# Optimization experiments

Measured on AMD Instinct MI355X. Metric: run time of the kernel, lower is better.

Reference implementation:

```python
import jax, jax.numpy as jnp
import numpy as np

HEADS = 8
DIM_HEAD = 8  # TransMIL passes heads as dim_head to NystromLayer
INNER = HEADS * DIM_HEAD  # 64
LANDMARKS = 256
PINV_ITERS = 6
HID = 512
IN_DIM = 1024
N_TOKENS = 19600


def layernorm(x, g, b, eps=1e-5):
    mu = x.mean(-1, keepdims=True)
    var = ((x - mu) ** 2).mean(-1, keepdims=True)
    return (x - mu) / jnp.sqrt(var + eps) * g + b


def moore_penrose_pinv(a, iters=PINV_ITERS):
    # a: [b, h, m, m]
    abs_a = jnp.abs(a)
    z = jnp.swapaxes(a, -1, -2) / (jnp.max(abs_a.sum(-1)) * jnp.max(abs_a.sum(-2)))
    I = jnp.eye(a.shape[-1], dtype=a.dtype)
    for _ in range(iters):
        az = a @ z
        z = 0.25 * z @ (13.0 * I - az @ (15.0 * I - az @ (7.0 * I - az)))
    return z


def dwconv2d(x, w, b, pad_h, pad_w):
    # x: [B,C,H,W], w: [C,1,kh,kw] depthwise
    y = jax.lax.conv_general_dilated(
        x, w, (1, 1), [(pad_h, pad_h), (pad_w, pad_w)],
        dimension_numbers=('NCHW', 'OIHW', 'NCHW'), feature_group_count=x.shape[1])
    if b is not None:
        y = y + b[None, :, None, None]
    return y


def nystrom_attention(x, qkv_w, out_w, out_b, res_w):
    b, n, _ = x.shape
    m = LANDMARKS
    pad = (m - n % m) % m
    xp = jnp.pad(x, ((0, 0), (pad, 0), (0, 0)))  # pad at the FRONT (as in lucidrains)
    n_p = n + pad
    qkv = xp @ qkv_w  # [b, n_p, 3*inner]
    q, k, v = jnp.split(qkv, 3, axis=-1)
    to_heads = lambda t: t.reshape(b, n_p, HEADS, DIM_HEAD).transpose(0, 2, 1, 3)
    q, k, v = to_heads(q), to_heads(k), to_heads(v)  # [b,h,n_p,d]
    q = q * (DIM_HEAD ** -0.5)
    l = n_p // m  # segment length per landmark
    q_l = q.reshape(b, HEADS, m, l, DIM_HEAD).mean(3)  # [b,h,m,d]
    k_l = k.reshape(b, HEADS, m, l, DIM_HEAD).mean(3)
    attn1 = jax.nn.softmax(jnp.einsum('bhid,bhjd->bhij', q, k_l), -1)    # [b,h,n_p,m]
    attn2 = jax.nn.softmax(jnp.einsum('bhid,bhjd->bhij', q_l, k_l), -1)  # [b,h,m,m]
    attn3 = jax.nn.softmax(jnp.einsum('bhid,bhjd->bhij', q_l, k), -1)    # [b,h,m,n_p]
    out = (attn1 @ moore_penrose_pinv(attn2)) @ (attn3 @ v)  # [b,h,n_p,d]
    # residual depthwise conv over sequence dim: Conv2d(heads, heads, (33,1), padding=(16,0), groups=heads)
    out = out + dwconv2d(v, res_w, None, 16, 0)
    out = out.transpose(0, 2, 1, 3).reshape(b, n_p, INNER)
    out = out @ out_w + out_b
    return out[:, -n:]


def ppeg(x, H, W, w7, b7, w5, b5, w3, b3):
    B, _, C = x.shape
    cls, feat = x[:, :1], x[:, 1:]
    f = feat.transpose(0, 2, 1).reshape(B, C, H, W)
    y = f + dwconv2d(f, w7, b7, 3, 3) + dwconv2d(f, w5, b5, 2, 2) + dwconv2d(f, w3, b3, 1, 1)
    y = y.reshape(B, C, H * W).transpose(0, 2, 1)
    return jnp.concatenate([cls, y], axis=1)


def transmil_forward(x, fc1_w, fc1_b, cls_token,
                     l1_norm_g, l1_norm_b, l1_qkv_w, l1_out_w, l1_out_b, l1_res_w,
                     l2_norm_g, l2_norm_b, l2_qkv_w, l2_out_w, l2_out_b, l2_res_w,
                     ppeg7_w, ppeg7_b, ppeg5_w, ppeg5_b, ppeg3_w, ppeg3_b,
                     norm_g, norm_b):
    h = jax.nn.gelu(x @ fc1_w + fc1_b, approximate=False)  # [1, N, HID]
    N = h.shape[1]
    side = int(np.ceil(np.sqrt(N)))
    add = side * side - N
    h = jnp.concatenate([h, h[:, :add]], axis=1)
    cls = jnp.broadcast_to(cls_token, (h.shape[0], 1, h.shape[2]))
    h = jnp.concatenate([cls, h], axis=1)
    h = h + nystrom_attention(layernorm(h, l1_norm_g, l1_norm_b), l1_qkv_w, l1_out_w, l1_out_b, l1_res_w)
    h = ppeg(h, side, side, ppeg7_w, ppeg7_b, ppeg5_w, ppeg5_b, ppeg3_w, ppeg3_b)
    h = h + nystrom_attention(layernorm(h, l2_norm_g, l2_norm_b), l2_qkv_w, l2_out_w, l2_out_b, l2_res_w)
    return layernorm(h, norm_g, norm_b)[:, 0]  # [1, HID]


def setup_inputs() -> dict:
    key = jax.random.key(0)
    ks = jax.random.split(key, 16)
    s = 0.02
    inp = {
        'x': jax.random.normal(ks[0], (1, N_TOKENS, IN_DIM), jnp.float32),
        'fc1_w': jax.random.normal(ks[1], (IN_DIM, HID), jnp.float32) * s,
        'fc1_b': jnp.zeros((HID,), jnp.float32),
        'cls_token': jax.random.normal(ks[2], (1, 1, HID), jnp.float32),
        'l1_norm_g': jnp.ones((HID,), jnp.float32),
        'l1_norm_b': jnp.zeros((HID,), jnp.float32),
        'l1_qkv_w': jax.random.normal(ks[3], (HID, 3 * INNER), jnp.float32) * s,
        'l1_out_w': jax.random.normal(ks[4], (INNER, HID), jnp.float32) * s,
        'l1_out_b': jnp.zeros((HID,), jnp.float32),
        'l1_res_w': jax.random.normal(ks[5], (HEADS, 1, 33, 1), jnp.float32) * 0.05,
        'l2_norm_g': jnp.ones((HID,), jnp.float32),
        'l2_norm_b': jnp.zeros((HID,), jnp.float32),
        'l2_qkv_w': jax.random.normal(ks[6], (HID, 3 * INNER), jnp.float32) * s,
        'l2_out_w': jax.random.normal(ks[7], (INNER, HID), jnp.float32) * s,
        'l2_out_b': jnp.zeros((HID,), jnp.float32),
        'l2_res_w': jax.random.normal(ks[8], (HEADS, 1, 33, 1), jnp.float32) * 0.05,
        'ppeg7_w': jax.random.normal(ks[9], (HID, 1, 7, 7), jnp.float32) * 0.05,
        'ppeg7_b': jnp.zeros((HID,), jnp.float32),
        'ppeg5_w': jax.random.normal(ks[10], (HID, 1, 5, 5), jnp.float32) * 0.05,
        'ppeg5_b': jnp.zeros((HID,), jnp.float32),
        'ppeg3_w': jax.random.normal(ks[11], (HID, 1, 3, 3), jnp.float32) * 0.05,
        'ppeg3_b': jnp.zeros((HID,), jnp.float32),
        'norm_g': jnp.ones((HID,), jnp.float32),
        'norm_b': jnp.zeros((HID,), jnp.float32),
    }
    return inp


def reference(x, fc1_w, fc1_b, cls_token,
              l1_norm_g, l1_norm_b, l1_qkv_w, l1_out_w, l1_out_b, l1_res_w,
              l2_norm_g, l2_norm_b, l2_qkv_w, l2_out_w, l2_out_b, l2_res_w,
              ppeg7_w, ppeg7_b, ppeg5_w, ppeg5_b, ppeg3_w, ppeg3_b,
              norm_g, norm_b):
    return transmil_forward(x, fc1_w, fc1_b, cls_token,
                            l1_norm_g, l1_norm_b, l1_qkv_w, l1_out_w, l1_out_b, l1_res_w,
                            l2_norm_g, l2_norm_b, l2_qkv_w, l2_out_w, l2_out_b, l2_res_w,
                            ppeg7_w, ppeg7_b, ppeg5_w, ppeg5_b, ppeg3_w, ppeg3_b,
                            norm_g, norm_b)
```

## Files before the change

### kernel.cpp

```cpp
#include <hip/hip_runtime.h>

namespace {

constexpr int NP   = 19712;
constexpr int NT   = 19601;
constexpr int NPIX = 19600;
constexpr int HD   = 512;
constexpr int ID   = 1024;
constexpr int NH   = 8;
constexpr int DH   = 8;
constexpr int NL   = 256;
constexpr int PADR = 111;
constexpr int SIDE = 140;
constexpr int CCH  = 128;
constexpr int PW   = 148;
constexpr int A3CHK = 256;
constexpr int A3NB  = NP / A3CHK;

typedef __attribute__((ext_vector_type(8))) short bf16x8;
typedef __attribute__((ext_vector_type(4))) float f32x4;

#define F4MAD(a, s, v) { (a).x += (s)*(v).x; (a).y += (s)*(v).y; (a).z += (s)*(v).z; (a).w += (s)*(v).w; }

#define GLOAD16(gptr, lptr) \
    __builtin_amdgcn_global_load_lds((const __attribute__((address_space(1))) void*)(gptr), \
                                     (__attribute__((address_space(3))) void*)(lptr), 16, 0, 0)

__device__ inline short f2bf(float f) {
    union { float f; unsigned u; } v; v.f = f;
    unsigned r = v.u + 0x7fffu + ((v.u >> 16) & 1u);
    return (short)(r >> 16);
}

__global__ void castX(const float* __restrict__ src, short* __restrict__ dst)
{
    size_t c = (size_t)blockIdx.x * 256 + threadIdx.x;
    const float4 x0 = *(const float4*)&src[c * 8];
    const float4 x1 = *(const float4*)&src[c * 8 + 4];
    bf16x8 p;
    p[0] = f2bf(x0.x); p[1] = f2bf(x0.y); p[2] = f2bf(x0.z); p[3] = f2bf(x0.w);
    p[4] = f2bf(x1.x); p[5] = f2bf(x1.y); p[6] = f2bf(x1.z); p[7] = f2bf(x1.w);
    *(bf16x8*)&dst[c * 8] = p;
}

__global__ void castT(const float* __restrict__ src, short* __restrict__ dst, int R, int C)
{
    __shared__ float t[32][33];
    const int tx = threadIdx.x & 31, ty = threadIdx.x >> 5;
    const int c0 = blockIdx.x * 32, r0 = blockIdx.y * 32;
    #pragma unroll
    for (int j = 0; j < 4; ++j)
        t[ty + 8 * j][tx] = src[(size_t)(r0 + ty + 8 * j) * C + c0 + tx];
    __syncthreads();
    #pragma unroll
    for (int j = 0; j < 4; ++j)
        dst[(size_t)(c0 + ty + 8 * j) * R + r0 + tx] = f2bf(t[tx][ty + 8 * j]);
}

__global__ __launch_bounds__(256) void gemm_fc1(const short* __restrict__ Xb,
                                                const short* __restrict__ Wt,
                                                const float* __restrict__ bias,
                                                float* __restrict__ out)
{
    __shared__ __align__(16) short As[2][128 * 32];
    __shared__ __align__(16) short Bs[2][128 * 32];
    const int tid  = threadIdx.x;
    const int col0 = blockIdx.x * 128;
    const int row0 = blockIdx.y * 128;
    const int wave = tid >> 6, lane = tid & 63;
    const int quad = lane >> 4, l16 = lane & 15;
    const int m_base = (wave >> 1) * 64, n_base = (wave & 1) * 64;
    const int kch = (quad ^ ((l16 >> 1) & 3)) * 8;
    f32x4 acc[4][4] = {};

    int    aldo[2];
    size_t agoff[2], bgoff[2];
    #pragma unroll
    for (int i = 0; i < 2; ++i) {
        int slot = i * 256 + wave * 64 + lane;
        int row  = slot >> 2;
        int g    = (slot & 3) ^ ((slot >> 3) & 3);
        aldo[i]  = slot * 8;
        agoff[i] = (size_t)(row0 + row) * ID + g * 8;
        bgoff[i] = (size_t)(col0 + row) * ID + g * 8;
    }
    auto stage = [&](int b, int k0) {
        #pragma unroll
        for (int i = 0; i < 2; ++i) {
            GLOAD16(&Xb[agoff[i] + k0], &As[b][aldo[i]]);
            GLOAD16(&Wt[bgoff[i] + k0], &Bs[b][aldo[i]]);
        }
    };

    stage(0, 0);
    __syncthreads();
    #pragma unroll 1
    for (int t = 0; t < 32; ++t) {
        const int cur = t & 1;
        if (t < 31) stage(cur ^ 1, (t + 1) * 32);
        bf16x8 af[4], bfr[4];
        #pragma unroll
        for (int i = 0; i < 4; ++i) {
            af[i]  = *(const bf16x8*)&As[cur][(m_base + i * 16 + l16) * 32 + kch];
            bfr[i] = *(const bf16x8*)&Bs[cur][(n_base + i * 16 + l16) * 32 + kch];
        }
        #pragma unroll
        for (int mi = 0; mi < 4; ++mi)
            #pragma unroll
            for (int ni = 0; ni < 4; ++ni)
                acc[mi][ni] = __builtin_amdgcn_mfma_f32_16x16x32_bf16(af[mi], bfr[ni], acc[mi][ni], 0, 0, 0);
        __syncthreads();
    }
    #pragma unroll
    for (int mi = 0; mi < 4; ++mi) {
        #pragma unroll
        for (int r = 0; r < 4; ++r) {
            int gr = row0 + m_base + mi * 16 + quad * 4 + r;
            if (gr >= NPIX) continue;
            #pragma unroll
            for (int ni = 0; ni < 4; ++ni) {
                int gc = col0 + n_base + ni * 16 + l16;
                float v = acc[mi][ni][r] + bias[gc];
                v = 0.5f * v * (1.f + erff(v * 0.70710678118654752f));
                out[(size_t)(gr + 1) * HD + gc] = v;
            }
        }
    }
}

__global__ __launch_bounds__(256) void gemm_qkv(const short* __restrict__ xpB,
                                                const short* __restrict__ Wt,
                                                float* __restrict__ qh,
                                                float* __restrict__ kh,
                                                float* __restrict__ vh)
{
    __shared__ __align__(16) short As[2][128 * 32];
    __shared__ __align__(16) short Bs[2][64 * 32];
    const int tid  = threadIdx.x;
    const int col0 = blockIdx.x * 64;
    const int row0 = blockIdx.y * 128;
    const int wave = tid >> 6, lane = tid & 63;
    const int quad = lane >> 4, l16 = lane & 15;
    const int m_base = (wave >> 1) * 64, n_base = (wave & 1) * 32;
    const int kch = (quad ^ ((l16 >> 1) & 3)) * 8;
    f32x4 acc[4][2] = {};

    int    aldo[2];
    size_t agoff[2];
    #pragma unroll
    for (int i = 0; i < 2; ++i) {
        int slot = i * 256 + wave * 64 + lane;
        int row  = slot >> 2;
        int g    = (slot & 3) ^ ((slot >> 3) & 3);
        aldo[i]  = slot * 8;
        agoff[i] = (size_t)(row0 + row) * HD + g * 8;
    }
    int bldo; size_t bgoff;
    {
        int slot = wave * 64 + lane;
        int row  = slot >> 2;
        int g    = (slot & 3) ^ ((slot >> 3) & 3);
        bldo  = slot * 8;
        bgoff = (size_t)(col0 + row) * HD + g * 8;
    }
    auto stage = [&](int b, int k0) {
        #pragma unroll
        for (int i = 0; i < 2; ++i)
            GLOAD16(&xpB[agoff[i] + k0], &As[b][aldo[i]]);
        GLOAD16(&Wt[bgoff + k0], &Bs[b][bldo]);
    };

    stage(0, 0);
    __syncthreads();
    #pragma unroll 1
    for (int t = 0; t < 16; ++t) {
        const int cur = t & 1;
        if (t < 15) stage(cur ^ 1, (t + 1) * 32);
        bf16x8 af[4], bfr[2];
        #pragma unroll
        for (int i = 0; i < 4; ++i)
            af[i] = *(const bf16x8*)&As[cur][(m_base + i * 16 + l16) * 32 + kch];
        #pragma unroll
        for (int i = 0; i < 2; ++i)
            bfr[i] = *(const bf16x8*)&Bs[cur][(n_base + i * 16 + l16) * 32 + kch];
        #pragma unroll
        for (int mi = 0; mi < 4; ++mi)
            #pragma unroll
            for (int ni = 0; ni < 2; ++ni)
                acc[mi][ni] = __builtin_amdgcn_mfma_f32_16x16x32_bf16(af[mi], bfr[ni], acc[mi][ni], 0, 0, 0);
        __syncthreads();
    }
    const int which = blockIdx.x;
    float* dst = (which == 0) ? qh : (which == 1) ? kh : vh;
    const float scale = (which == 0) ? 0.35355339059327373f : 1.f;
    #pragma unroll
    for (int mi = 0; mi < 4; ++mi) {
        #pragma unroll
        for (int r = 0; r < 4; ++r) {
            int gr = row0 + m_base + mi * 16 + quad * 4 + r;
            #pragma unroll
            for (int ni = 0; ni < 2; ++ni) {
                int n = n_base + ni * 16 + l16;
                int hh = n >> 3, d = n & 7;
                dst[((size_t)hh * NP + gr) * DH + d] = acc[mi][ni][r] * scale;
            }
        }
    }
}

__global__ void cls_init(const float* __restrict__ cls, float* __restrict__ h)
{
    int t = blockIdx.x * 256 + threadIdx.x;
    if (t < HD) h[t] = cls[t];
}

__global__ void copy512(const float* __restrict__ src, float* __restrict__ dst)
{
    dst[threadIdx.x] = src[threadIdx.x];
}

__global__ __launch_bounds__(256) void ln_pad(const float* __restrict__ h,
                                              const float* __restrict__ g,
                                              const float* __restrict__ b,
                                              short* __restrict__ xp)
{
    const int wave = threadIdx.x >> 6, lane = threadIdx.x & 63;
    const int row = blockIdx.x * 4 + wave;
    short* dst = xp + (size_t)row * HD + lane * 8;
    if (row < PADR) {
        bf16x8 z = {};
        *(bf16x8*)dst = z;
        return;
    }
    const float* src = h + (size_t)(row - PADR) * HD + lane * 8;
    float4 v0 = *(const float4*)src;
    float4 v1 = *(const float4*)(src + 4);
    float v[8] = {v0.x, v0.y, v0.z, v0.w, v1.x, v1.y, v1.z, v1.w};
    float s = 0.f;
    #pragma unroll
    for (int i = 0; i < 8; ++i) s += v[i];
    #pragma unroll
    for (int o = 1; o < 64; o <<= 1) s += __shfl_xor(s, o);
    float mu = s * (1.f / HD);
    float ss = 0.f;
    #pragma unroll
    for (int i = 0; i < 8; ++i) { float d = v[i] - mu; ss += d * d; }
    #pragma unroll
    for (int o = 1; o < 64; o <<= 1) ss += __shfl_xor(ss, o);
    float inv = rsqrtf(ss * (1.f / HD) + 1e-5f);
    float4 g0 = *(const float4*)&g[lane * 8];
    float4 g1 = *(const float4*)&g[lane * 8 + 4];
    float4 b0 = *(const float4*)&b[lane * 8];
    float4 b1 = *(const float4*)&b[lane * 8 + 4];
    float gg[8] = {g0.x, g0.y, g0.z, g0.w, g1.x, g1.y, g1.z, g1.w};
    float bb[8] = {b0.x, b0.y, b0.z, b0.w, b1.x, b1.y, b1.z, b1.w};
    bf16x8 o;
    #pragma unroll
    for (int i = 0; i < 8; ++i) o[i] = f2bf((v[i] - mu) * inv * gg[i] + bb[i]);
    *(bf16x8*)dst = o;
}

__global__ void landmarks(const float* __restrict__ qh, const float* __restrict__ kh,
                          float* __restrict__ ql, float* __restrict__ kl)
{
    int idx = blockIdx.x * 256 + threadIdx.x;
    int sel = idx >> 14;
    int rem = idx & 16383;
    int h = rem >> 11;
    int i = (rem >> 3) & 255;
    int d = rem & 7;
    const float* src = sel ? kh : qh;
    size_t base = ((size_t)h * NP + (size_t)i * 77) * DH + d;
    float s = 0.f;
    for (int j = 0; j < 77; ++j) s += src[base + (size_t)j * DH];
    (sel ? kl : ql)[((size_t)h * NL + i) * DH + d] = s * (1.f / 77.f);
}

__global__ void attn2_softmax(const float* __restrict__ ql, const float* __restrict__ kl,
                              float* __restrict__ a)
{
    const int i = blockIdx.x, h = blockIdx.y, j = threadIdx.x;
    __shared__ float sq[8];
    __shared__ float red[256];
    if (j < 8) sq[j] = ql[((size_t)h * NL + i) * DH + j];
    __syncthreads();
    const float* kr = kl + ((size_t)h * NL + j) * DH;
    float s = 0.f;
    #pragma unroll
    for (int d = 0; d < 8; ++d) s += sq[d] * kr[d];
    float e = __expf(s);
    red[j] = e;
    __syncthreads();
    for (int off = 128; off > 0; off >>= 1) {
        if (j < off) red[j] += red[j + off];
        __syncthreads();
    }
    a[((size_t)h * NL + i) * NL + j] = e / red[0];
}

__global__ void pinv_norms(const float* __restrict__ a, float* __restrict__ part)
{
    const int h = blockIdx.x & 7;
    const int mode = blockIdx.x >> 3;
    const int tid = threadIdx.x;
    const float* ah = a + (size_t)h * NL * NL;
    float s = 0.f;
    if (mode == 0) { for (int j = 0; j < NL; ++j) s += fabsf(ah[tid * NL + j]); }
    else           { for (int i = 0; i < NL; ++i) s += fabsf(ah[i * NL + tid]); }
    __shared__ float red[256];
    red[tid] = s;
    __syncthreads();
    for (int off = 128; off > 0; off >>= 1) {
        if (tid < off) red[tid] = fmaxf(red[tid], red[tid + off]);
        __syncthreads();
    }
    if (tid == 0) part[mode * 8 + h] = red[0];
}

__global__ void z0_init(const float* __restrict__ a, const float* __restrict__ part,
                        float* __restrict__ z)
{
    float s1 = part[0], s2 = part[8];
    #pragma unroll
    for (int h = 1; h < 8; ++h) { s1 = fmaxf(s1, part[h]); s2 = fmaxf(s2, part[8 + h]); }
    float inv = 1.f / (s1 * s2);
    int idx = blockIdx.x * 256 + threadIdx.x;
    int h = idx >> 16;
    int rem = idx & 65535;
    int i = rem >> 8, j = rem & 255;
    z[idx] = a[((size_t)h * NL + j) * NL + i] * inv;
}

__global__ void mm256(const float* __restrict__ A, const float* __restrict__ B,
                      float* __restrict__ D)
{
    const int h = blockIdx.z;
    const float* Ah = A + (size_t)h * NL * NL;
    const float* Bh = B + (size_t)h * NL * NL;
    float* Dh = D + (size_t)h * NL * NL;
    __shared__ __align__(16) float As[16][36];
    __shared__ __align__(16) float Bs[16][68];
    const int tid = threadIdx.x;
    const int tx = tid & 15, ty = tid >> 4;
    const int row0 = blockIdx.x * 32;
    const int col0 = blockIdx.y * 64;
    float acc[2][4] = {};
    const int ar = tid >> 3;
    const int ak = (tid & 7) * 2;
    const int bk = tid >> 4;
    const int bj = (tid & 15) * 4;
    for (int k0 = 0; k0 < NL; k0 += 16) {
        float2 av = *(const float2*)&Ah[(size_t)(row0 + ar) * NL + k0 + ak];
        As[ak][ar] = av.x; As[ak + 1][ar] = av.y;
        *(float4*)&Bs[bk][bj] = *(const float4*)&Bh[(size_t)(k0 + bk) * NL + col0 + bj];
        __syncthreads();
        #pragma unroll
        for (int k = 0; k < 16; ++k) {
            float2 a = *(const float2*)&As[k][ty * 2];
            float4 b = *(const float4*)&Bs[k][tx * 4];
            acc[0][0] += a.x * b.x; acc[0][1] += a.x * b.y; acc[0][2] += a.x * b.z; acc[0][3] += a.x * b.w;
            acc[1][0] += a.y * b.x; acc[1][1] += a.y * b.y; acc[1][2] += a.y * b.z; acc[1][3] += a.y * b.w;
        }
        __syncthreads();
    }
    #pragma unroll
    for (int r = 0; r < 2; ++r) {
        int gr = row0 + ty * 2 + r;
        #pragma unroll
        for (int c = 0; c < 4; ++c)
            Dh[(size_t)gr * NL + col0 + tx * 4 + c] = acc[r][c];
    }
}

__global__ __launch_bounds__(256) void mmF(const float* __restrict__ S,
                                           const float* __restrict__ w,
                                           float* __restrict__ wn,
                                           const float* __restrict__ yin,
                                           float* __restrict__ yout)
{
    const int h = blockIdx.z;
    const int tid = threadIdx.x;
    if (blockIdx.y == 4) {
        __shared__ float yL[NL * 9];
        __shared__ float tL[NL * 9];
        __shared__ float uL[NL * 9];
        const int s = blockIdx.x;
        const float* yh = yin + (size_t)h * NL * DH;
        #pragma unroll
        for (int i = 0; i < 8; ++i) {
            int idx = tid + 256 * i;
            yL[(idx >> 3) * 9 + (idx & 7)] = yh[idx];
        }
        __syncthreads();
        const float* wr = w + ((size_t)h * NL + tid) * NL;
        float t1[8] = {};
        for (int j = 0; j < NL; j += 4) {
            float4 wv = *(const float4*)&wr[j];
            #pragma unroll
            for (int d = 0; d < 8; ++d)
                t1[d] += wv.x * yL[j * 9 + d] + wv.y * yL[(j + 1) * 9 + d]
                       + wv.z * yL[(j + 2) * 9 + d] + wv.w * yL[(j + 3) * 9 + d];
        }
        #pragma unroll
        for (int d = 0; d < 8; ++d) {
            tL[tid * 9 + d] = t1[d];
            uL[tid * 9 + d] = 7.f * yL[tid * 9 + d] - t1[d];
        }
        __syncthreads();
        const int r = s * 32 + (tid >> 3), d = tid & 7;
        const float* Sr = S + ((size_t)h * NL + r) * NL;
        float acc = 13.f * yL[r * 9 + d] - 15.f * tL[r * 9 + d];
        for (int j = 0; j < NL; j += 4) {
            float4 sv = *(const float4*)&Sr[j];
            acc += sv.x * uL[j * 9 + d] + sv.y * uL[(j + 1) * 9 + d]
                 + sv.z * uL[(j + 2) * 9 + d] + sv.w * uL[(j + 3) * 9 + d];
        }
        yout[((size_t)h * NL + r) * DH + d] = acc;
        return;
    }
    const float* Sh = S + (size_t)h * NL * NL;
    const float* wh = w + (size_t)h * NL * NL;
    float* Dh = wn + (size_t)h * NL * NL;
    __shared__ __align__(16) float As[16][36];
    __shared__ __align__(16) float Bs[16][68];
    const int tx = tid & 15, ty = tid >> 4;
    const int row0 = blockIdx.x * 32;
    const int col0 = blockIdx.y * 64;
    float acc[2][4] = {};
    const int ar = tid >> 3;
    const int ak = (tid & 7) * 2;
    const int bk = tid >> 4;
    const int bj = (tid & 15) * 4;
    for (int k0 = 0; k0 < NL; k0 += 16) {
        float2 av = *(const float2*)&Sh[(size_t)(row0 + ar) * NL + k0 + ak];
        As[ak][ar] = av.x; As[ak + 1][ar] = av.y;
        size_t bo = (size_t)(k0 + bk) * NL + col0 + bj;
        float4 bw = *(const float4*)&wh[bo];
        float4 bs = *(const float4*)&Sh[bo];
        Bs[bk][bj]     = 7.f * bw.x - bs.x;
        Bs[bk][bj + 1] = 7.f * bw.y - bs.y;
        Bs[bk][bj + 2] = 7.f * bw.z - bs.z;
        Bs[bk][bj + 3] = 7.f * bw.w - bs.w;
        __syncthreads();
        #pragma unroll
        for (int k = 0; k < 16; ++k) {
            float2 a = *(const float2*)&As[k][ty * 2];
            float4 b = *(const float4*)&Bs[k][tx * 4];
            acc[0][0] += a.x * b.x; acc[0][1] += a.x * b.y; acc[0][2] += a.x * b.z; acc[0][3] += a.x * b.w;
            acc[1][0] += a.y * b.x; acc[1][1] += a.y * b.y; acc[1][2] += a.y * b.z; acc[1][3] += a.y * b.w;
        }
        __syncthreads();
    }
    #pragma unroll
    for (int r = 0; r < 2; ++r) {
        int gr = row0 + ty * 2 + r;
        #pragma unroll
        for (int c = 0; c < 4; ++c) {
            int gc = col0 + tx * 4 + c;
            size_t o = (size_t)gr * NL + gc;
            Dh[o] = 0.25f * (13.f * wh[o] - 15.f * Sh[o] + acc[r][c]);
        }
    }
}

__global__ __launch_bounds__(256) void yiter(const float* __restrict__ w,
                                             const float* __restrict__ S,
                                             const float* __restrict__ yin,
                                             float* __restrict__ yout)
{
    const int s = blockIdx.x, h = blockIdx.y, tid = threadIdx.x;
    __shared__ float yL[NL * 9];
    __shared__ float tL[NL * 9];
    __shared__ float uL[NL * 9];
    const float* yh = yin + (size_t)h * NL * DH;
    #pragma unroll
    for (int i = 0; i < 8; ++i) {
        int idx = tid + 256 * i;
        yL[(idx >> 3) * 9 + (idx & 7)] = yh[idx];
    }
    __syncthreads();
    const float* wr = w + ((size_t)h * NL + tid) * NL;
    float t1[8] = {};
    for (int j = 0; j < NL; j += 4) {
        float4 wv = *(const float4*)&wr[j];
        #pragma unroll
        for (int d = 0; d < 8; ++d)
            t1[d] += wv.x * yL[j * 9 + d] + wv.y * yL[(j + 1) * 9 + d]
                   + wv.z * yL[(j + 2) * 9 + d] + wv.w * yL[(j + 3) * 9 + d];
    }
    #pragma unroll
    for (int d = 0; d < 8; ++d) {
        tL[tid * 9 + d] = t1[d];
        uL[tid * 9 + d] = 7.f * yL[tid * 9 + d] - t1[d];
    }
    __syncthreads();
    const int r = s * 32 + (tid >> 3), d = tid & 7;
    const float* Sr = S + ((size_t)h * NL + r) * NL;
    float acc = 13.f * yL[r * 9 + d] - 15.f * tL[r * 9 + d];
    for (int j = 0; j < NL; j += 4) {
        float4 sv = *(const float4*)&Sr[j];
        acc += sv.x * uL[j * 9 + d] + sv.y * uL[(j + 1) * 9 + d]
             + sv.z * uL[(j + 2) * 9 + d] + sv.w * uL[(j + 3) * 9 + d];
    }
    yout[((size_t)h * NL + r) * DH + d] = acc;
}

__global__ void polyv(const float* __restrict__ M, const float* __restrict__ vin,
                      float* __restrict__ vout, float scale)
{
    const int h = blockIdx.y;
    __shared__ float vs[NL * DH];
    const int tid = threadIdx.x;
    const float* vh = vin + (size_t)h * NL * DH;
    #pragma unroll
    for (int i = 0; i < 8; ++i) vs[tid + 256 * i] = vh[tid + 256 * i];
    __syncthreads();
    const int row = blockIdx.x * 32 + (tid >> 3);
    const int d = tid & 7;
    const float* Mr = M + ((size_t)h * NL + row) * NL;
    float acc = 0.f;
    #pragma unroll 4
    for (int j = 0; j < NL; j += 4) {
        float4 m = *(const float4*)&Mr[j];
        acc += m.x * vs[j * 8 + d]      + m.y * vs[j * 8 + 8 + d]
             + m.z * vs[j * 8 + 16 + d] + m.w * vs[j * 8 + 24 + d];
    }
    vout[((size_t)h * NL + row) * DH + d] = acc * scale;
}

__global__ __launch_bounds__(256) void attn3v(const float* __restrict__ kh,
                                              const float* __restrict__ vh,
                                              const float* __restrict__ ql,
                                              float* __restrict__ part)
{
    const int ck = blockIdx.x, h = blockIdx.y, tid = threadIdx.x;
    __shared__ __align__(16) float4 kv[A3CHK][4];
    const float* kb = kh + ((size_t)h * NP + (size_t)ck * A3CHK) * DH;
    const float* vb = vh + ((size_t)h * NP + (size_t)ck * A3CHK) * DH;
    #pragma unroll
    for (int i = 0; i < 2; ++i) {
        int idx = tid + 256 * i;
        int t = idx >> 1, p = idx & 1;
        kv[t][p]     = *(const float4*)&kb[t * 8 + p * 4];
        kv[t][2 + p] = *(const float4*)&vb[t * 8 + p * 4];
    }
    float q[8];
    const float* qp = ql + ((size_t)h * NL + tid) * DH;
    #pragma unroll
    for (int d = 0; d < 8; ++d) q[d] = qp[d];
    __syncthreads();
    float den = 0.f;
    float4 a0 = make_float4(0.f, 0.f, 0.f, 0.f);
    float4 a1 = make_float4(0.f, 0.f, 0.f, 0.f);
    #pragma unroll 4
    for (int t = 0; t < A3CHK; ++t) {
        float4 k0 = kv[t][0], k1 = kv[t][1];
        float s = q[0] * k0.x + q[1] * k0.y + q[2] * k0.z + q[3] * k0.w
                + q[4] * k1.x + q[5] * k1.y + q[6] * k1.z + q[7] * k1.w;
        float e = __expf(s);
        den += e;
        float4 v0 = kv[t][2], v1 = kv[t][3];
        F4MAD(a0, e, v0); F4MAD(a1, e, v1);
    }
    float* p = part + (((size_t)h * A3NB + ck) * NL + tid) * 9;
    p[0] = den;
    p[1] = a0.x; p[2] = a0.y; p[3] = a0.z; p[4] = a0.w;
    p[5] = a1.x; p[6] = a1.y; p[7] = a1.z; p[8] = a1.w;
}

__global__ void attn3v_merge(const float* __restrict__ part, float* __restrict__ y)
{
    const int h = blockIdx.x, i = threadIdx.x;
    float den = 0.f;
    float acc[8] = {};
    for (int ck = 0; ck < A3NB; ++ck) {
        const float* p = part + (((size_t)h * A3NB + ck) * NL + i) * 9;
        den += p[0];
        #pragma unroll
        for (int d = 0; d < 8; ++d) acc[d] += p[1 + d];
    }
    float inv = 1.f / den;
    #pragma unroll
    for (int d = 0; d < 8; ++d) y[((size_t)h * NL + i) * DH + d] = acc[d] * inv;
}

__global__ __launch_bounds__(256) void attn1_conv(const float* __restrict__ qh,
                                                  const float* __restrict__ vh,
                                                  const float* __restrict__ klg,
                                                  const float* __restrict__ zwg,
                                                  const float* __restrict__ rw,
                                                  float* __restrict__ aout)
{
    const int h = blockIdx.y;
    __shared__ __align__(16) float kl[NL * DH];
    __shared__ __align__(16) float zw[NL * DH];
    const int tid = threadIdx.x;
    #pragma unroll
    for (int q = 0; q < 8; ++q) {
        kl[tid + 256 * q] = klg[(size_t)h * NL * DH + tid + 256 * q];
        zw[tid + 256 * q] = zwg[(size_t)h * NL * DH + tid + 256 * q];
    }
    __syncthreads();
    const int r = blockIdx.x * 256 + tid;
    if (r >= NT) return;
    const int t = r + PADR;
    const float* qp = qh + ((size_t)h * NP + t) * DH;
    float4 q0 = *(const float4*)qp;
    float4 q1 = *(const float4*)(qp + 4);
    float den = 0.f;
    float4 acc0 = make_float4(0.f, 0.f, 0.f, 0.f);
    float4 acc1 = make_float4(0.f, 0.f, 0.f, 0.f);
    #pragma unroll 4
    for (int i = 0; i < NL; ++i) {
        float4 k0 = *(const float4*)&kl[i * 8];
        float4 k1 = *(const float4*)&kl[i * 8 + 4];
        float s = q0.x * k0.x + q0.y * k0.y + q0.z * k0.z + q0.w * k0.w
                + q1.x * k1.x + q1.y * k1.y + q1.z * k1.z + q1.w * k1.w;
        float e = __expf(s);
        den += e;
        float4 z0 = *(const float4*)&zw[i * 8];
        float4 z1 = *(const float4*)&zw[i * 8 + 4];
        F4MAD(acc0, e, z0); F4MAD(acc1, e, z1);
    }
    float inv = 1.f / den;
    const float* vb = vh + (size_t)h * NP * DH;
    float4 c0 = make_float4(0.f, 0.f, 0.f, 0.f);
    float4 c1 = make_float4(0.f, 0.f, 0.f, 0.f);
    #pragma unroll
    for (int j = 0; j < 33; ++j) {
        int tp = t - 16 + j;
        if (tp >= NP) continue;
        float wv = rw[h * 33 + j];
        float4 v0 = *(const float4*)&vb[(size_t)tp * 8];
        float4 v1 = *(const float4*)&vb[(size_t)tp * 8 + 4];
        F4MAD(c0, wv, v0); F4MAD(c1, wv, v1);
    }
    float* op = aout + (size_t)r * 64 + h * 8;
    *(float4*)op = make_float4(acc0.x * inv + c0.x, acc0.y * inv + c0.y,
                               acc0.z * inv + c0.z, acc0.w * inv + c0.w);
    *(float4*)(op + 4) = make_float4(acc1.x * inv + c1.x, acc1.y * inv + c1.y,
                                     acc1.z * inv + c1.z, acc1.w * inv + c1.w);
}

__global__ void outproj(const float* __restrict__ aout, const float* __restrict__ W,
                        const float* __restrict__ bias, float* __restrict__ h)
{
    const int r0 = blockIdx.x * 16;
    const int tid = threadIdx.x;
    __shared__ float ao[16][64];
    #pragma unroll
    for (int s = 0; s < 2; ++s) {
        int idx = tid + s * 512;
        int rr = idx >> 6, kk = idx & 63;
        int gr = r0 + rr;
        ao[rr][kk] = (gr < NT) ? aout[(size_t)gr * 64 + kk] : 0.f;
    }
    __syncthreads();
    float acc[16] = {};
    for (int k = 0; k < 64; ++k) {
        float wv = W[(size_t)k * HD + tid];
        #pragma unroll
        for (int r = 0; r < 16; ++r) acc[r] += ao[r][k] * wv;
    }
    float bv = bias[tid];
    #pragma unroll
    for (int r = 0; r < 16; ++r) {
        int gr = r0 + r;
        if (gr < NT) h[(size_t)gr * HD + tid] += acc[r] + bv;
    }
}

__global__ void ppeg_wprep(const float* __restrict__ w7, const float* __restrict__ b7,
                           const float* __restrict__ w5, const float* __restrict__ b5,
                           const float* __restrict__ w3, const float* __restrict__ b3,
                           float* __restrict__ wc, float* __restrict__ bsum)
{
    int idx = blockIdx.x * 256 + threadIdx.x;
    if (idx < HD * 49) {
        int c = idx / 49, t = idx - c * 49;
        int dy = t / 7 - 3, dx = t % 7 - 3;
        float v = w7[idx];
        if (dy >= -2 && dy <= 2 && dx >= -2 && dx <= 2) v += w5[c * 25 + (dy + 2) * 5 + (dx + 2)];
        if (dy >= -1 && dy <= 1 && dx >= -1 && dx <= 1) v += w3[c * 9 + (dy + 1) * 3 + (dx + 1)];
        if (t == 24) v += 1.f;
        wc[idx] = v;
    } else if (idx < HD * 49 + HD) {
        int c = idx - HD * 49;
        bsum[c] = b7[c] + b5[c] + b3[c];
    }
}

__global__ void ppeg_t1(const float* __restrict__ hin, float* __restrict__ plan, int ch0)
{
    __shared__ float tile[32][33];
    const int tx = threadIdx.x & 31, ty = threadIdx.x >> 5;
    const int p0 = blockIdx.x * 32;
    const int c0 = ch0 + blockIdx.y * 32;
    #pragma unroll
    for (int j = 0; j < 4; ++j) {
        int p = p0 + ty + j * 8;
        tile[ty + j * 8][tx] = (p < NPIX) ? hin[(size_t)(1 + p) * HD + c0 + tx] : 0.f;
    }
    __syncthreads();
    #pragma unroll
    for (int j = 0; j < 4; ++j) {
        int p = p0 + tx;
        int cc = ty + j * 8;
        if (p < NPIX) plan[(size_t)(blockIdx.y * 32 + cc) * NPIX + p] = tile[tx][cc];
    }
}

__global__ __launch_bounds__(256) void ppeg_conv(const float* __restrict__ plan,
                                                 const float* __restrict__ wc,
                                                 float* __restrict__ plan2, int ch0)
{
    __shared__ __align__(16) float img[41 * PW];
    const int tid = threadIdx.x;
    const int cl = blockIdx.x;
    const int yq = blockIdx.y;
    for (int i = tid; i < 41 * PW; i += 256) img[i] = 0.f;
    __syncthreads();
    const float* src = plan + (size_t)cl * NPIX;
    for (int i = tid; i < 41 * SIDE; i += 256) {
        int ly = i / SIDE, x = i - ly * SIDE;
        int y = yq * 35 - 3 + ly;
        if (y >= 0 && y < SIDE) img[ly * PW + x + 3] = src[y * SIDE + x];
    }
    const float* w = wc + (size_t)(ch0 + cl) * 49;
    float wr[49];
    #pragma unroll
    for (int t = 0; t < 49; ++t) wr[t] = w[t];
    __syncthreads();
    float* dst = plan2 + (size_t)cl * NPIX;
    for (int g = tid; g < 35 * 35; g += 256) {
        int yl = g / 35, x0 = (g - yl * 35) * 4;
        float acc0 = 0.f, acc1 = 0.f, acc2 = 0.f, acc3 = 0.f;
        #pragma unroll
        for (int a = 0; a < 7; ++a) {
            const float* row = &img[(yl + a) * PW + x0];
            float4 A = *(const float4*)(row);
            float4 B = *(const float4*)(row + 4);
            float4 C = *(const float4*)(row + 8);
            float e0 = A.x, e1 = A.y, e2 = A.z, e3 = A.w;
            float e4 = B.x, e5 = B.y, e6 = B.z, e7 = B.w;
            float e8 = C.x, e9 = C.y;
            const float w0 = wr[a*7+0], w1 = wr[a*7+1], w2 = wr[a*7+2], w3v = wr[a*7+3];
            const float w4 = wr[a*7+4], w5v = wr[a*7+5], w6 = wr[a*7+6];
            acc0 += w0*e0 + w1*e1 + w2*e2 + w3v*e3 + w4*e4 + w5v*e5 + w6*e6;
            acc1 += w0*e1 + w1*e2 + w2*e3 + w3v*e4 + w4*e5 + w5v*e6 + w6*e7;
            acc2 += w0*e2 + w1*e3 + w2*e4 + w3v*e5 + w4*e6 + w5v*e7 + w6*e8;
            acc3 += w0*e3 + w1*e4 + w2*e5 + w3v*e6 + w4*e7 + w5v*e8 + w6*e9;
        }
        *(float4*)&dst[(yq * 35 + yl) * SIDE + x0] = make_float4(acc0, acc1, acc2, acc3);
    }
}

__global__ void ppeg_t2(const float* __restrict__ plan2, const float* __restrict__ bsum,
                        float* __restrict__ hout, int ch0)
{
    __shared__ float tile[32][33];
    const int tx = threadIdx.x & 31, ty = threadIdx.x >> 5;
    const int p0 = blockIdx.x * 32;
    #pragma unroll
    for (int j = 0; j < 4; ++j) {
        int p = p0 + tx;
        int cc = ty + j * 8;
        tile[tx][cc] = (p < NPIX) ? plan2[(size_t)(blockIdx.y * 32 + cc) * NPIX + p] : 0.f;
    }
    __syncthreads();
    const int c0 = ch0 + blockIdx.y * 32;
    float bv = bsum[c0 + tx];
    #pragma unroll
    for (int j = 0; j < 4; ++j) {
        int p = p0 + ty + j * 8;
        if (p < NPIX) hout[(size_t)(1 + p) * HD + c0 + tx] = tile[ty + j * 8][tx] + bv;
    }
}

__global__ void final_ln(const float* __restrict__ h, const float* __restrict__ g,
                         const float* __restrict__ b, float* __restrict__ out)
{
    const int tid = threadIdx.x;
    float v0 = h[tid], v1 = h[tid + 256];
    __shared__ float red[256];
    red[tid] = v0 + v1;
    __syncthreads();
    for (int off = 128; off > 0; off >>= 1) {
        if (tid < off) red[tid] += red[tid + off];
        __syncthreads();
    }
    float mu = red[0] * (1.f / HD);
    __syncthreads();
    float d0 = v0 - mu, d1 = v1 - mu;
    red[tid] = d0 * d0 + d1 * d1;
    __syncthreads();
    for (int off = 128; off > 0; off >>= 1) {
        if (tid < off) red[tid] += red[tid + off];
        __syncthreads();
    }
    float inv = rsqrtf(red[0] * (1.f / HD) + 1e-5f);
    out[tid]       = d0 * inv * g[tid] + b[tid];
    out[tid + 256] = d1 * inv * g[tid + 256] + b[tid + 256];
}

}

extern "C" void kernel_launch(void* const* d_in, const int* in_sizes, int n_in,
                              void* d_out, int out_size, void* d_ws, size_t ws_size,
                              hipStream_t stream)
{
    const float* x      = (const float*)d_in[0];
    const float* fc1_w  = (const float*)d_in[1];
    const float* fc1_b  = (const float*)d_in[2];
    const float* cls    = (const float*)d_in[3];
    const float* l1_g   = (const float*)d_in[4];
    const float* l1_bb  = (const float*)d_in[5];
    const float* l1_qkv = (const float*)d_in[6];
    const float* l1_ow  = (const float*)d_in[7];
    const float* l1_ob  = (const float*)d_in[8];
    const float* l1_rw  = (const float*)d_in[9];
    const float* l2_g   = (const float*)d_in[10];
    const float* l2_bb  = (const float*)d_in[11];
    const float* l2_qkv = (const float*)d_in[12];
    const float* l2_ow  = (const float*)d_in[13];
    const float* l2_ob  = (const float*)d_in[14];
    const float* l2_rw  = (const float*)d_in[15];
    const float* p7w    = (const float*)d_in[16];
    const float* p7b    = (const float*)d_in[17];
    const float* p5w    = (const float*)d_in[18];
    const float* p5b    = (const float*)d_in[19];
    const float* p3w    = (const float*)d_in[20];
    const float* p3b    = (const float*)d_in[21];
    const float* ng     = (const float*)d_in[22];
    const float* nb     = (const float*)d_in[23];
    float* out = (float*)d_out;

    char* ws = (char*)d_ws;
    size_t off = 0;
    auto alloc = [&](size_t bytes) {
        char* p = ws + off;
        off += (bytes + 255) & ~(size_t)255;
        return (void*)p;
    };
    float* bufA = (float*)alloc((size_t)NP * HD * 4);
    float* bufB = (float*)alloc((size_t)NP * HD * 4);
    float* qh   = (float*)alloc((size_t)NH * NP * DH * 4);
    float* kh   = (float*)alloc((size_t)NH * NP * DH * 4);
    float* vh   = (float*)alloc((size_t)NH * NP * DH * 4);
    float* aout = (float*)alloc((size_t)NP * 64 * 4);
    float* ql   = (float*)alloc((size_t)NH * NL * DH * 4);
    float* klm  = (float*)alloc((size_t)NH * NL * DH * 4);
    float* ybuf = (float*)alloc((size_t)NH * NL * DH * 4);
    float* ybuf2= (float*)alloc((size_t)NH * NL * DH * 4);
    float* zwb  = (float*)alloc((size_t)NH * NL * DH * 4);
    float* a2   = (float*)alloc((size_t)NH * NL * NL * 4);
    float* zb0  = (float*)alloc((size_t)NH * NL * NL * 4);
    float* azb  = (float*)alloc((size_t)NH * NL * NL * 4);
    float* tb   = (float*)alloc((size_t)NH * NL * NL * 4);
    float* ub   = (float*)alloc((size_t)NH * NL * NL * 4);
    float* part = (float*)alloc(256);
    float* a3p  = (float*)alloc((size_t)NH * A3NB * NL * 9 * 4);
    float* plan  = (float*)alloc((size_t)CCH * NPIX * 4);
    float* plan2 = (float*)alloc((size_t)CCH * NPIX * 4);
    float* wcomb = (float*)alloc((size_t)HD * 49 * 4);
    float* bsum  = (float*)alloc((size_t)HD * 4);
    short* wt1   = (short*)alloc((size_t)HD * ID * 2);
    short* wtq   = (short*)alloc((size_t)192 * HD * 2);
    short* xb    = (short*)alloc((size_t)NP * ID * 2);
    short* xpB   = (short*)alloc((size_t)NP * HD * 2);
    (void)ws_size; (void)in_sizes; (void)n_in; (void)out_size;

    castX<<<(NPIX * ID / 8) / 256, 256, 0, stream>>>(x, xb);
    castT<<<dim3(HD / 32, ID / 32), 256, 0, stream>>>(fc1_w, wt1, ID, HD);
    gemm_fc1<<<dim3(4, 154), 256, 0, stream>>>(xb, wt1, fc1_b, bufA);
    cls_init<<<2, 256, 0, stream>>>(cls, bufA);

    auto attention = [&](float* hbuf, const float* lg, const float* lb,
                         const float* qkvw, const float* ow, const float* ob,
                         const float* rw) {
        ln_pad<<<NP / 4, 256, 0, stream>>>(hbuf, lg, lb, xpB);
        castT<<<dim3(192 / 32, HD / 32), 256, 0, stream>>>(qkvw, wtq, HD, 192);
        gemm_qkv<<<dim3(3, 154), 256, 0, stream>>>(xpB, wtq, qh, kh, vh);
        landmarks<<<128, 256, 0, stream>>>(qh, kh, ql, klm);
        attn2_softmax<<<dim3(NL, NH), 256, 0, stream>>>(ql, klm, a2);
        pinv_norms<<<16, 256, 0, stream>>>(a2, part);
        z0_init<<<2048, 256, 0, stream>>>(a2, part, zb0);
        attn3v<<<dim3(A3NB, NH), 256, 0, stream>>>(kh, vh, ql, a3p);
        attn3v_merge<<<NH, 256, 0, stream>>>(a3p, ybuf);
        mm256<<<dim3(8, 4, 8), 256, 0, stream>>>(a2, zb0, azb);
        float* wc = azb;
        float* wn = tb;
        float* yc = ybuf;
        float* yn = ybuf2;
        for (int it = 0; it < 6; ++it) {
            mm256<<<dim3(8, 4, 8), 256, 0, stream>>>(wc, wc, ub);
            if (it < 5) {
                mmF<<<dim3(8, 5, 8), 256, 0, stream>>>(ub, wc, wn, yc, yn);
                { float* t = yc; yc = yn; yn = t; }
                { float* t = wc; wc = wn; wn = t; }
            } else {
                yiter<<<dim3(8, 8), 256, 0, stream>>>(wc, ub, yc, yn);
                { float* t = yc; yc = yn; yn = t; }
            }
        }
        polyv<<<dim3(8, NH), 256, 0, stream>>>(zb0, yc, zwb, 2.44140625e-4f);
        attn1_conv<<<dim3(77, NH), 256, 0, stream>>>(qh, vh, klm, zwb, rw, aout);
        outproj<<<(NT + 15) / 16, 512, 0, stream>>>(aout, ow, ob, hbuf);
    };

    attention(bufA, l1_g, l1_bb, l1_qkv, l1_ow, l1_ob, l1_rw);

    ppeg_wprep<<<(HD * 49 + HD + 255) / 256, 256, 0, stream>>>(p7w, p7b, p5w, p5b, p3w, p3b,
                                                               wcomb, bsum);
    copy512<<<1, 512, 0, stream>>>(bufA, bufB);
    constexpr int PTILES = (NPIX + 31) / 32;
    for (int ch0 = 0; ch0 < HD; ch0 += CCH) {
        ppeg_t1<<<dim3(PTILES, CCH / 32), 256, 0, stream>>>(bufA, plan, ch0);
        ppeg_conv<<<dim3(CCH, 4), 256, 0, stream>>>(plan, wcomb, plan2, ch0);
        ppeg_t2<<<dim3(PTILES, CCH / 32), 256, 0, stream>>>(plan2, bsum, bufB, ch0);
    }

    attention(bufB, l2_g, l2_bb, l2_qkv, l2_ow, l2_ob, l2_rw);
    final_ln<<<1, 256, 0, stream>>>(bufB, ng, nb, out);
}
```

Before: 1.158 ms.

## Compute PPEG conv directly in token-major layout and parallelize attn3v merge

Replaces the transpose-to-planar, convolve, transpose-back PPEG pipeline (12 launches over 4 channel chunks) with a single kernel that tiles 16x16 pixels by 16 channels, loads a haloed tile straight from the token-major buffer into shared memory, and writes results back in place. This removes two full-tensor transposes and the planar scratch buffers. The attn3v merge is also spread over 8x more blocks, one thread per (landmark, dim), to raise parallelism in that small reduction. The halo tile re-reads about 90% extra input, and the merge now loads the denominator redundantly in each of the 8 threads sharing a landmark.

```diff
diff --git a/kernel.cpp b/kernel.cpp
--- a/kernel.cpp
+++ b/kernel.cpp
@@ -12,15 +12,18 @@
 constexpr int NL   = 256;
 constexpr int PADR = 111;
 constexpr int SIDE = 140;
-constexpr int CCH  = 128;
-constexpr int PW   = 148;
 constexpr int A3CHK = 256;
 constexpr int A3NB  = NP / A3CHK;
 
+constexpr int PTW = 16, PTH = 16, PCC = 16;
+constexpr int PHW = PTW + 6, PHH = PTH + 6;
+constexpr int PSLOT = 20;
+
 typedef __attribute__((ext_vector_type(8))) short bf16x8;
 typedef __attribute__((ext_vector_type(4))) float f32x4;
 
 #define F4MAD(a, s, v) { (a).x += (s)*(v).x; (a).y += (s)*(v).y; (a).z += (s)*(v).z; (a).w += (s)*(v).w; }
+#define F4FMA(a, ww, v) { (a).x += (ww).x*(v).x; (a).y += (ww).y*(v).y; (a).z += (ww).z*(v).z; (a).w += (ww).w*(v).w; }
 
 #define GLOAD16(gptr, lptr) \
     __builtin_amdgcn_global_load_lds((const __attribute__((address_space(1))) void*)(gptr), \
@@ -570,18 +573,17 @@
 
 __global__ void attn3v_merge(const float* __restrict__ part, float* __restrict__ y)
 {
-    const int h = blockIdx.x, i = threadIdx.x;
-    float den = 0.f;
-    float acc[8] = {};
+    const int h = blockIdx.x;
+    const int i = blockIdx.y * 32 + (threadIdx.x >> 3);
+    const int d = threadIdx.x & 7;
+    float acc = 0.f, den = 0.f;
+    const float* p = part + ((size_t)h * A3NB * NL + i) * 9;
     for (int ck = 0; ck < A3NB; ++ck) {
-        const float* p = part + (((size_t)h * A3NB + ck) * NL + i) * 9;
-        den += p[0];
-        #pragma unroll
-        for (int d = 0; d < 8; ++d) acc[d] += p[1 + d];
-    }
-    float inv = 1.f / den;
-    #pragma unroll
-    for (int d = 0; d < 8; ++d) y[((size_t)h * NL + i) * DH + d] = acc[d] * inv;
+        const float* q = p + (size_t)ck * NL * 9;
+        den += q[0];
+        acc += q[1 + d];
+    }
+    y[((size_t)h * NL + i) * DH + d] = acc / den;
 }
 
 __global__ __launch_bounds__(256) void attn1_conv(const float* __restrict__ qh,
@@ -690,90 +692,60 @@
     }
 }
 
-__global__ void ppeg_t1(const float* __restrict__ hin, float* __restrict__ plan, int ch0)
-{
-    __shared__ float tile[32][33];
-    const int tx = threadIdx.x & 31, ty = threadIdx.x >> 5;
-    const int p0 = blockIdx.x * 32;
-    const int c0 = ch0 + blockIdx.y * 32;
-    #pragma unroll
-    for (int j = 0; j < 4; ++j) {
-        int p = p0 + ty + j * 8;
-        tile[ty + j * 8][tx] = (p < NPIX) ? hin[(size_t)(1 + p) * HD + c0 + tx] : 0.f;
-    }
-    __syncthreads();
-    #pragma unroll
-    for (int j = 0; j < 4; ++j) {
-        int p = p0 + tx;
-        int cc = ty + j * 8;
-        if (p < NPIX) plan[(size_t)(blockIdx.y * 32 + cc) * NPIX + p] = tile[tx][cc];
-    }
-}
-
-__global__ __launch_bounds__(256) void ppeg_conv(const float* __restrict__ plan,
-                                                 const float* __restrict__ wc,
-                                                 float* __restrict__ plan2, int ch0)
-{
-    __shared__ __align__(16) float img[41 * PW];
+__global__ __launch_bounds__(256) void ppeg_direct(const float* __restrict__ hin,
+                                                   const float* __restrict__ wc,
+                                                   const float* __restrict__ bsum,
+                                                   float* __restrict__ hout)
+{
+    __shared__ __align__(16) float in_sh[PHH * PHW * PSLOT];
+    __shared__ float wL[49 * PCC];
     const int tid = threadIdx.x;
-    const int cl = blockIdx.x;
-    const int yq = blockIdx.y;
-    for (int i = tid; i < 41 * PW; i += 256) img[i] = 0.f;
-    __syncthreads();
-    const float* src = plan + (size_t)cl * NPIX;
-    for (int i = tid; i < 41 * SIDE; i += 256) {
-        int ly = i / SIDE, x = i - ly * SIDE;
-        int y = yq * 35 - 3 + ly;
-        if (y >= 0 && y < SIDE) img[ly * PW + x + 3] = src[y * SIDE + x];
-    }
-    const float* w = wc + (size_t)(ch0 + cl) * 49;
-    float wr[49];
-    #pragma unroll
-    for (int t = 0; t < 49; ++t) wr[t] = w[t];
-    __syncthreads();
-    float* dst = plan2 + (size_t)cl * NPIX;
-    for (int g = tid; g < 35 * 35; g += 256) {
-        int yl = g / 35, x0 = (g - yl * 35) * 4;
-        float acc0 = 0.f, acc1 = 0.f, acc2 = 0.f, acc3 = 0.f;
-        #pragma unroll
-        for (int a = 0; a < 7; ++a) {
-            const float* row = &img[(yl + a) * PW + x0];
-            float4 A = *(const float4*)(row);
-            float4 B = *(const float4*)(row + 4);
-            float4 C = *(const float4*)(row + 8);
-            float e0 = A.x, e1 = A.y, e2 = A.z, e3 = A.w;
-            float e4 = B.x, e5 = B.y, e6 = B.z, e7 = B.w;
-            float e8 = C.x, e9 = C.y;
-            const float w0 = wr[a*7+0], w1 = wr[a*7+1], w2 = wr[a*7+2], w3v = wr[a*7+3];
-            const float w4 = wr[a*7+4], w5v = wr[a*7+5], w6 = wr[a*7+6];
-            acc0 += w0*e0 + w1*e1 + w2*e2 + w3v*e3 + w4*e4 + w5v*e5 + w6*e6;
-            acc1 += w0*e1 + w1*e2 + w2*e3 + w3v*e4 + w4*e5 + w5v*e6 + w6*e7;
-            acc2 += w0*e2 + w1*e3 + w2*e4 + w3v*e5 + w4*e6 + w5v*e7 + w6*e8;
-            acc3 += w0*e3 + w1*e4 + w2*e5 + w3v*e6 + w4*e7 + w5v*e8 + w6*e9;
-        }
-        *(float4*)&dst[(yq * 35 + yl) * SIDE + x0] = make_float4(acc0, acc1, acc2, acc3);
-    }
-}
-
-__global__ void ppeg_t2(const float* __restrict__ plan2, const float* __restrict__ bsum,
-                        float* __restrict__ hout, int ch0)
-{
-    __shared__ float tile[32][33];
-    const int tx = threadIdx.x & 31, ty = threadIdx.x >> 5;
-    const int p0 = blockIdx.x * 32;
-    #pragma unroll
-    for (int j = 0; j < 4; ++j) {
-        int p = p0 + tx;
-        int cc = ty + j * 8;
-        tile[tx][cc] = (p < NPIX) ? plan2[(size_t)(blockIdx.y * 32 + cc) * NPIX + p] : 0.f;
-    }
-    __syncthreads();
-    const int c0 = ch0 + blockIdx.y * 32;
-    float bv = bsum[c0 + tx];
-    #pragma unroll
-    for (int j = 0; j < 4; ++j) {
-        int p = p0 + ty + j * 8;
-        if (p < NPIX) hout[(size_t)(1 + p) * HD + c0 + tx] = tile[ty + j * 8][tx] + bv;
+    const int tx0 = blockIdx.x * PTW;
+    const int ty0 = blockIdx.y * PTH;
+    const int c0  = blockIdx.z * PCC;
+    for (int i = tid; i < 49 * PCC; i += 256) {
+        int c = i / 49, tap = i - c * 49;
+        wL[tap * PCC + c] = wc[(size_t)(c0 + c) * 49 + tap];
+    }
+    for (int idx = tid; idx < PHH * PHW * 4; idx += 256) {
+        int pos = idx >> 2, q = idx & 3;
+        int ly = pos / PHW, lx = pos - ly * PHW;
+        int gy = ty0 - 3 + ly, gx = tx0 - 3 + lx;
+        float4 v = make_float4(0.f, 0.f, 0.f, 0.f);
+        if (gy >= 0 && gy < SIDE && gx >= 0 && gx < SIDE)
+            v = *(const float4*)&hin[(size_t)(1 + gy * SIDE + gx) * HD + c0 + q * 4];
+        *(float4*)&in_sh[pos * PSLOT + q * 4] = v;
+    }
+    __syncthreads();
+    const int y  = tid >> 4;
+    const int x4 = (tid >> 2) & 3;
+    const int c4 = tid & 3;
+    const int xb = x4 * 4;
+    float4 acc[4] = {make_float4(0.f,0.f,0.f,0.f), make_float4(0.f,0.f,0.f,0.f),
+                     make_float4(0.f,0.f,0.f,0.f), make_float4(0.f,0.f,0.f,0.f)};
+    #pragma unroll 1
+    for (int dy = 0; dy < 7; ++dy) {
+        float4 row[10];
+        #pragma unroll
+        for (int k = 0; k < 10; ++k)
+            row[k] = *(const float4*)&in_sh[((y + dy) * PHW + xb + k) * PSLOT + c4 * 4];
+        #pragma unroll
+        for (int dx = 0; dx < 7; ++dx) {
+            float4 wv = *(const float4*)&wL[(dy * 7 + dx) * PCC + c4 * 4];
+            #pragma unroll
+            for (int xi = 0; xi < 4; ++xi) F4FMA(acc[xi], wv, row[xi + dx]);
+        }
+    }
+    const int gy = ty0 + y;
+    if (gy >= SIDE) return;
+    float4 bv = *(const float4*)&bsum[c0 + c4 * 4];
+    #pragma unroll
+    for (int xi = 0; xi < 4; ++xi) {
+        int gx = tx0 + xb + xi;
+        if (gx >= SIDE) continue;
+        float4 o = make_float4(acc[xi].x + bv.x, acc[xi].y + bv.y,
+                               acc[xi].z + bv.z, acc[xi].w + bv.w);
+        *(float4*)&hout[(size_t)(1 + gy * SIDE + gx) * HD + c0 + c4 * 4] = o;
     }
 }
 
@@ -860,8 +832,6 @@
     float* ub   = (float*)alloc((size_t)NH * NL * NL * 4);
     float* part = (float*)alloc(256);
     float* a3p  = (float*)alloc((size_t)NH * A3NB * NL * 9 * 4);
-    float* plan  = (float*)alloc((size_t)CCH * NPIX * 4);
-    float* plan2 = (float*)alloc((size_t)CCH * NPIX * 4);
     float* wcomb = (float*)alloc((size_t)HD * 49 * 4);
     float* bsum  = (float*)alloc((size_t)HD * 4);
     short* wt1   = (short*)alloc((size_t)HD * ID * 2);
@@ -886,7 +856,7 @@
         pinv_norms<<<16, 256, 0, stream>>>(a2, part);
         z0_init<<<2048, 256, 0, stream>>>(a2, part, zb0);
         attn3v<<<dim3(A3NB, NH), 256, 0, stream>>>(kh, vh, ql, a3p);
-        attn3v_merge<<<NH, 256, 0, stream>>>(a3p, ybuf);
+        attn3v_merge<<<dim3(NH, 8), 256, 0, stream>>>(a3p, ybuf);
         mm256<<<dim3(8, 4, 8), 256, 0, stream>>>(a2, zb0, azb);
         float* wc = azb;
         float* wn = tb;
@@ -913,12 +883,8 @@
     ppeg_wprep<<<(HD * 49 + HD + 255) / 256, 256, 0, stream>>>(p7w, p7b, p5w, p5b, p3w, p3b,
                                                                wcomb, bsum);
     copy512<<<1, 512, 0, stream>>>(bufA, bufB);
-    constexpr int PTILES = (NPIX + 31) / 32;
-    for (int ch0 = 0; ch0 < HD; ch0 += CCH) {
-        ppeg_t1<<<dim3(PTILES, CCH / 32), 256, 0, stream>>>(bufA, plan, ch0);
-        ppeg_conv<<<dim3(CCH, 4), 256, 0, stream>>>(plan, wcomb, plan2, ch0);
-        ppeg_t2<<<dim3(PTILES, CCH / 32), 256, 0, stream>>>(plan2, bsum, bufB, ch0);
-    }
+    ppeg_direct<<<dim3((SIDE + PTW - 1) / PTW, (SIDE + PTH - 1) / PTH, HD / PCC),
+                  256, 0, stream>>>(bufA, wcomb, bsum, bufB);
 
     attention(bufB, l2_g, l2_bb, l2_qkv, l2_ow, l2_ob, l2_rw);
     final_ln<<<1, 256, 0, stream>>>(bufB, ng, nb, out);
```

Measured after the change: 1.032 ms. 1.12x faster.
